# Kernel tuning notes

Hardware: AMD Instinct MI355X
Metric: run time of the kernel (lower is better)

Reference implementation:

```python
import jax, jax.numpy as jnp
import numpy as np

BATCH = 2
SEQ = 2048
DIM = 2048
HEADS = 16
DIM_HEAD = 64
DIM_INNER = HEADS * DIM_HEAD  # 1024
SOFTCAP = 50.0
EPS = 1e-12


def setup_inputs() -> dict:
    key = jax.random.key(0)
    k1, k2, k3, k4 = jax.random.split(key, 4)
    x = jax.random.normal(k1, (BATCH, SEQ, DIM), dtype=jnp.float32)
    # RMSNorm gamma param (initialized near zero in the torch module)
    gamma = jax.random.normal(k2, (DIM,), dtype=jnp.float32) * 0.02
    # Linear weights stored already-transposed: x @ W
    w_qkv = jax.random.normal(k3, (DIM, 3 * DIM_INNER), dtype=jnp.float32) * (DIM ** -0.5)
    w_out = jax.random.normal(k4, (DIM_INNER, DIM), dtype=jnp.float32) * (DIM_INNER ** -0.5)
    # (type, offset, length) triples per batch; bidirectional attention inside each span
    modalities = jnp.array(
        [[[0, 256, 256], [0, 1024, 512]],
         [[0, 128, 256], [0, 1536, 384]]], dtype=jnp.int32)
    return dict(x=x, gamma=gamma, w_qkv=w_qkv, w_out=w_out, modalities=modalities)


def _transfusion_attn_mask(seq_len, modalities):
    # causal | (q in span AND kv in span)  -> Bool[b, i, j]
    seq = jnp.arange(seq_len)
    causal = seq[:, None] >= seq[None, :]                      # [i, j]
    offsets = modalities[..., 1]                                # [b, m]
    ends = offsets + modalities[..., 2]                         # [b, m]
    q_in = seq[None, None, :] >= offsets[..., None]             # [b, m, i]
    kv_in = seq[None, None, :] < ends[..., None]                # [b, m, j]
    is_modality = jnp.any(q_in[..., :, None] & kv_in[..., None, :], axis=1)  # [b, i, j]
    return causal[None] | is_modality


def _rmsnorm(x, gamma):
    n = jnp.sqrt(jnp.sum(x * x, axis=-1, keepdims=True))
    x = x / jnp.maximum(n, EPS)
    return x * (DIM ** 0.5) * (gamma + 1.0)


def reference(x, gamma, w_qkv, w_out, modalities):
    xn = _rmsnorm(x, gamma)
    qkv = xn @ w_qkv                                            # [b, n, 3*h*d]
    qkv = qkv.reshape(BATCH, SEQ, 3, HEADS, DIM_HEAD)
    qkv = jnp.transpose(qkv, (2, 0, 3, 1, 4))                   # [3, b, h, n, d]
    q, k, v = qkv[0], qkv[1], qkv[2]
    q = q * (DIM_HEAD ** -0.5)
    sim = jnp.einsum('bhid,bhjd->bhij', q, k)
    sim = jnp.tanh(sim / SOFTCAP) * SOFTCAP                     # softclamp
    mask = _transfusion_attn_mask(SEQ, modalities)              # [b, i, j]
    neg = -jnp.finfo(sim.dtype).max
    sim = jnp.where(mask[:, None, :, :], sim, neg)
    attn = jax.nn.softmax(sim, axis=-1)
    out = jnp.einsum('bhij,bhjd->bhid', attn, v)
    out = jnp.transpose(out, (0, 2, 1, 3)).reshape(BATCH, SEQ, DIM_INNER)
    return out @ w_out
```

## Files before the change

### kernel.cpp

```cpp
#include <hip/hip_runtime.h>
#include <hip/hip_bf16.h>

typedef unsigned short u16;
typedef unsigned int u32;
typedef __attribute__((ext_vector_type(8))) short short8;
typedef __attribute__((ext_vector_type(4))) float f32x4;
typedef __attribute__((ext_vector_type(4))) u16 u16x4;

#define DEV __device__ __forceinline__

DEV u16 f2bf(float f) {
    union { float f; u32 u; } v; v.f = f;
    u32 r = v.u;
    u32 lsb = (r >> 16) & 1u;
    r += 0x7fffu + lsb;
    return (u16)(r >> 16);
}

DEV void gload_lds16(const u16* g, u16* l) {
    __builtin_amdgcn_global_load_lds(
        (const __attribute__((address_space(1))) u32*)(const void*)g,
        (__attribute__((address_space(3))) u32*)(void*)l,
        16, 0, 0);
}

__global__ void prep(const float* __restrict__ x, const float* __restrict__ gamma,
                     const float* __restrict__ w_qkv, const float* __restrict__ w_out,
                     u16* __restrict__ xn, u16* __restrict__ wqkvT, u16* __restrict__ woutT) {
    __shared__ float tile[32][33];
    __shared__ float red[4];
    int id = blockIdx.x;
    int t = threadIdx.x;
    if (id < 8192) {
        const float* in; u16* out; int R, C, bx, by;
        if (id < 6144) { in = w_qkv; out = wqkvT; R = 2048; C = 3072; bx = id % 96; by = id / 96; }
        else { id -= 6144; in = w_out; out = woutT; R = 1024; C = 2048; bx = id % 64; by = id / 64; }
        int tx = t & 31, ty = t >> 5;
        int c0 = bx * 32, r0 = by * 32;
#pragma unroll
        for (int i = 0; i < 4; i++)
            tile[ty * 4 + i][tx] = in[(size_t)(r0 + ty * 4 + i) * C + c0 + tx];
        __syncthreads();
#pragma unroll
        for (int i = 0; i < 4; i++)
            out[(size_t)(c0 + ty * 4 + i) * R + r0 + tx] = f2bf(tile[tx][ty * 4 + i]);
    } else {
        int row = id - 8192;
        const float4* xr = (const float4*)(x + (size_t)row * 2048);
        float4 a = xr[t];
        float4 b = xr[256 + t];
        float ss = a.x * a.x + a.y * a.y + a.z * a.z + a.w * a.w +
                   b.x * b.x + b.y * b.y + b.z * b.z + b.w * b.w;
#pragma unroll
        for (int off = 32; off; off >>= 1) ss += __shfl_xor(ss, off);
        if ((t & 63) == 0) red[t >> 6] = ss;
        __syncthreads();
        float tot = red[0] + red[1] + red[2] + red[3];
        float n = sqrtf(tot);
        float inv = 45.254833995939045f / fmaxf(n, 1e-12f);
        const float4* gr = (const float4*)gamma;
        float4 g0 = gr[t], g1 = gr[256 + t];
        u16x4 o0 = { f2bf(a.x * inv * (g0.x + 1.f)), f2bf(a.y * inv * (g0.y + 1.f)),
                     f2bf(a.z * inv * (g0.z + 1.f)), f2bf(a.w * inv * (g0.w + 1.f)) };
        u16x4 o1 = { f2bf(b.x * inv * (g1.x + 1.f)), f2bf(b.y * inv * (g1.y + 1.f)),
                     f2bf(b.z * inv * (g1.z + 1.f)), f2bf(b.w * inv * (g1.w + 1.f)) };
        u16x4* xo = (u16x4*)(xn + (size_t)row * 2048);
        xo[t] = o0;
        xo[256 + t] = o1;
    }
}

template <int EPI, int CCOL>
__global__ __launch_bounds__(512, 1) void gemm8f(
    const u16* __restrict__ A, const u16* __restrict__ BT,
    int M, int N, int K,
    float* __restrict__ Cout,
    u16* __restrict__ qb, u16* __restrict__ kb, u16* __restrict__ vT) {
    __shared__ __align__(16) u16 As[2][2][8192];
    __shared__ __align__(16) u16 Bs[2][2][8192];
    int t = threadIdx.x, lane = t & 63, wid = t >> 6;
    int g = lane >> 4, r = lane & 15;
    int wm = wid >> 2, wn = wid & 3;
    int rsw = r & 7;

    int id = blockIdx.x;
    int xcd = id & 7, slot = id >> 3;
    int by = (xcd >> 1) * 4 + slot / CCOL;
    int bx = (xcd & 1) * CCOL + slot % CCOL;
    int brow = by * 256, bcol = bx * 256;

    int gsl = (t & 7) ^ ((t >> 3) & 7);
    const u16* AgH = A + (size_t)(brow + (t >> 3)) * K + gsl * 8;
    const u16* BgH = BT + (size_t)(bcol + (t >> 3)) * K + gsl * 8;
    const size_t loK = (size_t)128 * K, r64K = (size_t)64 * K;
    int dstc = t * 8;

    f32x4 acc[2][4][2][2] = {};
    int NT = K >> 6;

#define STG_AH(bf_, kt_) { gload_lds16(AgH + (kt_) * 64, &As[bf_][0][dstc]); \
                           gload_lds16(AgH + r64K + (kt_) * 64, &As[bf_][0][dstc + 4096]); }
#define STG_AL(bf_, kt_) { gload_lds16(AgH + loK + (kt_) * 64, &As[bf_][1][dstc]); \
                           gload_lds16(AgH + loK + r64K + (kt_) * 64, &As[bf_][1][dstc + 4096]); }
#define STG_BH(bf_, kt_) { gload_lds16(BgH + (kt_) * 64, &Bs[bf_][0][dstc]); \
                           gload_lds16(BgH + r64K + (kt_) * 64, &Bs[bf_][0][dstc + 4096]); }
#define STG_BL(bf_, kt_) { gload_lds16(BgH + loK + (kt_) * 64, &Bs[bf_][1][dstc]); \
                           gload_lds16(BgH + loK + r64K + (kt_) * 64, &Bs[bf_][1][dstc + 4096]); }
#define READ_A(qm_) { \
    _Pragma("unroll") for (int mf = 0; mf < 4; mf++) \
    _Pragma("unroll") for (int ks = 0; ks < 2; ks++) \
        areg[mf][ks] = *(const short8*)&As[buf][qm_][(wm * 64 + mf * 16 + r) * 64 + (((ks << 2) + g) ^ rsw) * 8]; }
#define READ_B(qn_) { \
    _Pragma("unroll") for (int nf = 0; nf < 2; nf++) \
    _Pragma("unroll") for (int ks = 0; ks < 2; ks++) \
        breg[qn_][nf][ks] = *(const short8*)&Bs[buf][qn_][(wn * 32 + nf * 16 + r) * 64 + (((ks << 2) + g) ^ rsw) * 8]; }
#define PHASE_MFMA(qm_, qn_) { \
    __builtin_amdgcn_s_setprio(1); \
    _Pragma("unroll") for (int ks = 0; ks < 2; ks++) \
    _Pragma("unroll") for (int mf = 0; mf < 4; mf++) \
    _Pragma("unroll") for (int nf = 0; nf < 2; nf++) \
        acc[qm_][mf][qn_][nf] = __builtin_amdgcn_mfma_f32_16x16x32_bf16( \
            areg[mf][ks], breg[qn_][nf][ks], acc[qm_][mf][qn_][nf], 0, 0, 0); \
    __builtin_amdgcn_s_setprio(0); }
#define LGKM0() asm volatile("s_waitcnt lgkmcnt(0)" ::: "memory")
#define BAR() __builtin_amdgcn_s_barrier()

    STG_AH(0, 0); STG_AL(0, 0); STG_BH(0, 0); STG_BL(0, 0);
    asm volatile("s_waitcnt vmcnt(4)" ::: "memory");
    if (NT > 1) { STG_AH(1, 1); STG_AL(1, 1); STG_BH(1, 1); }
    asm volatile("s_waitcnt vmcnt(6)" ::: "memory");
    BAR();

    for (int kt = 0; kt < NT; ++kt) {
        int buf = kt & 1, ob = buf ^ 1;
        bool s1 = kt + 1 < NT, s2 = kt + 2 < NT;
        short8 areg[4][2], breg[2][2][2];

        READ_B(0); READ_A(0);
        if (s1) STG_BL(ob, kt + 1);
        BAR(); LGKM0();
        PHASE_MFMA(0, 0);
        BAR();

        READ_B(1);
        if (s2) STG_AH(buf, kt + 2);
        BAR(); LGKM0();
        PHASE_MFMA(0, 1);
        BAR();

        READ_A(1);
        if (s2) STG_AL(buf, kt + 2);
        BAR(); LGKM0();
        PHASE_MFMA(1, 0);
        BAR();

        if (s2) STG_BH(buf, kt + 2);
        PHASE_MFMA(1, 1);
        if (s2) { asm volatile("s_waitcnt vmcnt(6)" ::: "memory"); }
        else    { asm volatile("s_waitcnt vmcnt(0)" ::: "memory"); }
        BAR();
    }
#undef STG_AH
#undef STG_AL
#undef STG_BH
#undef STG_BL
#undef READ_A
#undef READ_B
#undef PHASE_MFMA
#undef LGKM0
#undef BAR

    if (EPI == 0) {
#pragma unroll
        for (int qm = 0; qm < 2; qm++)
#pragma unroll
            for (int mf = 0; mf < 4; mf++)
#pragma unroll
                for (int qn = 0; qn < 2; qn++)
#pragma unroll
                    for (int nf = 0; nf < 2; nf++) {
                        int cb = bcol + qn * 128 + wn * 32 + nf * 16 + r;
                        int which = cb >> 10;
                        int hd = cb & 1023;
                        int hh = hd >> 6, d = hd & 63;
#pragma unroll
                        for (int j = 0; j < 4; j++) {
                            int rr = brow + qm * 128 + wm * 64 + mf * 16 + 4 * g + j;
                            int b = rr >> 11, nn = rr & 2047;
                            float v = acc[qm][mf][qn][nf][j];
                            size_t bh = (size_t)(b * 16 + hh);
                            if (which == 0)      qb[(bh * 2048 + nn) * 64 + d] = f2bf(v * 0.125f);
                            else if (which == 1) kb[(bh * 2048 + nn) * 64 + d] = f2bf(v);
                            else                 vT[(bh * 64 + d) * 2048 + nn] = f2bf(v);
                        }
                    }
    } else {
#pragma unroll
        for (int qm = 0; qm < 2; qm++)
#pragma unroll
            for (int mf = 0; mf < 4; mf++)
#pragma unroll
                for (int qn = 0; qn < 2; qn++)
#pragma unroll
                    for (int nf = 0; nf < 2; nf++) {
                        int cb = bcol + qn * 128 + wn * 32 + nf * 16 + r;
#pragma unroll
                        for (int j = 0; j < 4; j++) {
                            int rr = brow + qm * 128 + wm * 64 + mf * 16 + 4 * g + j;
                            Cout[(size_t)rr * N + cb] = acc[qm][mf][qn][nf][j];
                        }
                    }
    }
}

__global__ __launch_bounds__(256, 3) void flash_attn(
    const u16* __restrict__ q, const u16* __restrict__ kk, const u16* __restrict__ vT,
    const int* __restrict__ mods, u16* __restrict__ attn_out) {
    __shared__ __align__(16) u16 Ks[2][4096];
    __shared__ __align__(16) u16 Vs[2][4096];
    __shared__ __align__(16) u16 Plds[4][16][72];
    int t = threadIdx.x, lane = t & 63, wave = t >> 6;
    int g = lane >> 4, r = lane & 15;
    int h = blockIdx.x, b = blockIdx.y;
    int qs = (31 - blockIdx.z) * 64;
    int bh = b * 16 + h;
    int qbase = qs + wave * 16;

    int off0 = mods[b * 6 + 1], end0 = off0 + mods[b * 6 + 2];
    int off1 = mods[b * 6 + 4], end1 = off1 + mods[b * 6 + 5];

    const u16* Qp = q + ((size_t)bh * 2048 + qbase) * 64;
    short8 qf0 = *(const short8*)(Qp + (size_t)r * 64 + 8 * g);
    short8 qf1 = *(const short8*)(Qp + (size_t)r * 64 + 32 + 8 * g);

    int iq = qbase + r;
    int lim0 = (iq >= off0) ? end0 : 0;
    int lim1 = (iq >= off1) ? end1 : 0;
    int rowlim = max(iq + 1, max(lim0, lim1));

    int jlb = qs + 64;
    if (qs + 63 >= off0) jlb = max(jlb, end0);
    if (qs + 63 >= off1) jlb = max(jlb, end1);

    const u16* Kp = kk + (size_t)bh * 2048 * 64;
    const u16* Vp = vT + (size_t)bh * 64 * 2048;
    u16* Pw = &Plds[wave][0][0];

    f32x4 ot[4] = {};
    float psA = 0.f, psB = 0.f;
    int sw = r & 7;

    auto stage64 = [&](const u16* gbase, int gstride, u16* lds) {
#pragma unroll
        for (int i = 0; i < 2; i++) {
            int c = i * 256 + t;
            int row = c >> 3;
            int gsl = (c & 7) ^ (row & 7);
            gload_lds16(gbase + (size_t)row * gstride + 8 * gsl,
                        lds + (size_t)(c & ~63) * 8);
        }
    };

    stage64(Kp, 64, Ks[0]);
    stage64(Vp, 2048, Vs[0]);
    int buf = 0;

    for (int jb = 0; jb < jlb; jb += 64) {
        if (jb + 64 < jlb) {
            stage64(Kp + (size_t)(jb + 64) * 64, 64, Ks[buf ^ 1]);
            stage64(Vp + (jb + 64), 2048, Vs[buf ^ 1]);
            asm volatile("s_waitcnt vmcnt(4)" ::: "memory");
        } else {
            asm volatile("s_waitcnt vmcnt(0)" ::: "memory");
        }
        __builtin_amdgcn_s_barrier();
        const u16* Kt = Ks[buf];
        const u16* Vt = Vs[buf];

        f32x4 st[4];
#pragma unroll
        for (int tt = 0; tt < 4; tt++) {
            int row = 16 * tt + r;
            short8 kf0 = *(const short8*)&Kt[(size_t)(row * 8 + (g ^ sw)) * 8];
            short8 kf1 = *(const short8*)&Kt[(size_t)(row * 8 + ((4 + g) ^ sw)) * 8];
            f32x4 z = {};
            z = __builtin_amdgcn_mfma_f32_16x16x32_bf16(kf0, qf0, z, 0, 0, 0);
            z = __builtin_amdgcn_mfma_f32_16x16x32_bf16(kf1, qf1, z, 0, 0, 0);
            st[tt] = z;
        }
#pragma unroll
        for (int tt = 0; tt < 4; tt++) {
            int kvb = jb + 16 * tt + 4 * g;
            float p0, p1, p2, p3;
#pragma unroll
            for (int j = 0; j < 4; j++) {
                float x = st[tt][j];
                float x2 = x * x;
                float inner = __builtin_fmaf(x2, 2.1333333e-8f, -1.3333333e-4f);
                float poly = __builtin_fmaf(x2, inner, 1.0f);
                float pv = __expf(x * poly);
                pv = (kvb + j < rowlim) ? pv : 0.f;
                if (j == 0) p0 = pv; else if (j == 1) p1 = pv;
                else if (j == 2) p2 = pv; else p3 = pv;
            }
            psA += p0 + p1;
            psB += p2 + p3;
            u32 pk0, pk1;
            asm("v_cvt_pk_bf16_f32 %0, %1, %2" : "=v"(pk0) : "v"(p0), "v"(p1));
            asm("v_cvt_pk_bf16_f32 %0, %1, %2" : "=v"(pk1) : "v"(p2), "v"(p3));
            *(u32*)&Pw[r * 72 + 16 * tt + 4 * g] = pk0;
            *(u32*)&Pw[r * 72 + 16 * tt + 4 * g + 2] = pk1;
        }
        short8 pf0 = *(const short8*)&Pw[r * 72 + 8 * g];
        short8 pf1 = *(const short8*)&Pw[r * 72 + 32 + 8 * g];
#pragma unroll
        for (int dt = 0; dt < 4; dt++) {
            int row = 16 * dt + r;
            short8 vf0 = *(const short8*)&Vt[(size_t)(row * 8 + (g ^ sw)) * 8];
            short8 vf1 = *(const short8*)&Vt[(size_t)(row * 8 + ((4 + g) ^ sw)) * 8];
            ot[dt] = __builtin_amdgcn_mfma_f32_16x16x32_bf16(vf0, pf0, ot[dt], 0, 0, 0);
            ot[dt] = __builtin_amdgcn_mfma_f32_16x16x32_bf16(vf1, pf1, ot[dt], 0, 0, 0);
        }
        asm volatile("s_waitcnt lgkmcnt(0)" ::: "memory");
        __builtin_amdgcn_s_barrier();
        buf ^= 1;
    }

    float lrow = psA + psB;
    lrow += __shfl_xor(lrow, 16);
    lrow += __shfl_xor(lrow, 32);
    float inv = 1.f / lrow;
    u16* Op = attn_out + ((size_t)(b * 2048 + qbase + r)) * 1024 + h * 64;
#pragma unroll
    for (int dt = 0; dt < 4; dt++) {
        u16x4 o = { f2bf(ot[dt][0] * inv), f2bf(ot[dt][1] * inv),
                    f2bf(ot[dt][2] * inv), f2bf(ot[dt][3] * inv) };
        *(u16x4*)(Op + dt * 16 + 4 * g) = o;
    }
}

extern "C" void kernel_launch(void* const* d_in, const int* in_sizes, int n_in,
                              void* d_out, int out_size, void* d_ws, size_t ws_size,
                              hipStream_t stream) {
    const float* x = (const float*)d_in[0];
    const float* gamma = (const float*)d_in[1];
    const float* w_qkv = (const float*)d_in[2];
    const float* w_out = (const float*)d_in[3];
    const int* mods = (const int*)d_in[4];
    float* out = (float*)d_out;

    u16* ws = (u16*)d_ws;
    u16* xn    = ws;
    u16* wqkvT = ws + 8388608;
    u16* woutT = ws + 14680064;
    u16* qb    = ws + 16777216;
    u16* kb    = ws + 20971520;
    u16* vT    = ws + 25165824;
    u16* ao    = ws + 29360128;

    prep<<<dim3(12288), dim3(256), 0, stream>>>(x, gamma, w_qkv, w_out, xn, wqkvT, woutT);
    gemm8f<0, 6><<<dim3(192), dim3(512), 0, stream>>>(xn, wqkvT, 4096, 3072, 2048,
                                                      nullptr, qb, kb, vT);
    flash_attn<<<dim3(16, 2, 32), dim3(256), 0, stream>>>(qb, kb, vT, mods, ao);
    gemm8f<1, 4><<<dim3(128), dim3(512), 0, stream>>>(ao, woutT, 4096, 2048, 1024,
                                                      out, nullptr, nullptr, nullptr);
}
```

Measured before the change: 177.5 us.

## Double-buffer GEMM register fragments to overlap LDS reads with MFMA

Restructures the GEMM main loop to ping-pong A/B register fragments (a0/a1, b0/b1). The next quarter's LDS reads are issued before the current MFMA phase, with partial lgkmcnt waits in place of full drains. This removes one barrier per phase and prefetches the next k-tile's first fragments during the last MFMA phase. The cost is higher register pressure, plus correctness that now depends on hand-tuned waitcnt counts and moved global-to-LDS staging points.

```diff
diff --git a/kernel.cpp b/kernel.cpp
--- a/kernel.cpp
+++ b/kernel.cpp
@@ -71,7 +71,7 @@
 }
 
 template <int EPI, int CCOL>
-__global__ __launch_bounds__(512, 1) void gemm8f(
+__global__ __launch_bounds__(512, 1) void gemmpp(
     const u16* __restrict__ A, const u16* __restrict__ BT,
     int M, int N, int K,
     float* __restrict__ Cout,
@@ -96,6 +96,7 @@
     int dstc = t * 8;
 
     f32x4 acc[2][4][2][2] = {};
+    short8 a0[4][2], a1[4][2], b0[2][2], b1[2][2];
     int NT = K >> 6;
 
 #define STG_AH(bf_, kt_) { gload_lds16(AgH + (kt_) * 64, &As[bf_][0][dstc]); \
@@ -106,68 +107,72 @@
                            gload_lds16(BgH + r64K + (kt_) * 64, &Bs[bf_][0][dstc + 4096]); }
 #define STG_BL(bf_, kt_) { gload_lds16(BgH + loK + (kt_) * 64, &Bs[bf_][1][dstc]); \
                            gload_lds16(BgH + loK + r64K + (kt_) * 64, &Bs[bf_][1][dstc + 4096]); }
-#define READ_A(qm_) { \
+#define RD_A(dst_, bb_, hh_) { \
     _Pragma("unroll") for (int mf = 0; mf < 4; mf++) \
     _Pragma("unroll") for (int ks = 0; ks < 2; ks++) \
-        areg[mf][ks] = *(const short8*)&As[buf][qm_][(wm * 64 + mf * 16 + r) * 64 + (((ks << 2) + g) ^ rsw) * 8]; }
-#define READ_B(qn_) { \
+        dst_[mf][ks] = *(const short8*)&As[bb_][hh_][(wm * 64 + mf * 16 + r) * 64 + (((ks << 2) + g) ^ rsw) * 8]; }
+#define RD_B(dst_, bb_, hh_) { \
     _Pragma("unroll") for (int nf = 0; nf < 2; nf++) \
     _Pragma("unroll") for (int ks = 0; ks < 2; ks++) \
-        breg[qn_][nf][ks] = *(const short8*)&Bs[buf][qn_][(wn * 32 + nf * 16 + r) * 64 + (((ks << 2) + g) ^ rsw) * 8]; }
-#define PHASE_MFMA(qm_, qn_) { \
+        dst_[nf][ks] = *(const short8*)&Bs[bb_][hh_][(wn * 32 + nf * 16 + r) * 64 + (((ks << 2) + g) ^ rsw) * 8]; }
+#define MFMA_Q(qm_, qn_, aa_, bb_) { \
     __builtin_amdgcn_s_setprio(1); \
     _Pragma("unroll") for (int ks = 0; ks < 2; ks++) \
     _Pragma("unroll") for (int mf = 0; mf < 4; mf++) \
     _Pragma("unroll") for (int nf = 0; nf < 2; nf++) \
         acc[qm_][mf][qn_][nf] = __builtin_amdgcn_mfma_f32_16x16x32_bf16( \
-            areg[mf][ks], breg[qn_][nf][ks], acc[qm_][mf][qn_][nf], 0, 0, 0); \
+            aa_[mf][ks], bb_[nf][ks], acc[qm_][mf][qn_][nf], 0, 0, 0); \
     __builtin_amdgcn_s_setprio(0); }
-#define LGKM0() asm volatile("s_waitcnt lgkmcnt(0)" ::: "memory")
+#define SCHEDB() __builtin_amdgcn_sched_barrier(0)
 #define BAR() __builtin_amdgcn_s_barrier()
 
     STG_AH(0, 0); STG_AL(0, 0); STG_BH(0, 0); STG_BL(0, 0);
-    asm volatile("s_waitcnt vmcnt(4)" ::: "memory");
     if (NT > 1) { STG_AH(1, 1); STG_AL(1, 1); STG_BH(1, 1); }
     asm volatile("s_waitcnt vmcnt(6)" ::: "memory");
+    SCHEDB();
     BAR();
+    RD_A(a0, 0, 0);
+    RD_B(b0, 0, 0);
 
     for (int kt = 0; kt < NT; ++kt) {
         int buf = kt & 1, ob = buf ^ 1;
         bool s1 = kt + 1 < NT, s2 = kt + 2 < NT;
-        short8 areg[4][2], breg[2][2][2];
-
-        READ_B(0); READ_A(0);
+
+        RD_B(b1, buf, 1);
         if (s1) STG_BL(ob, kt + 1);
-        BAR(); LGKM0();
-        PHASE_MFMA(0, 0);
+        asm volatile("s_waitcnt lgkmcnt(4)" ::: "memory");
+        SCHEDB();
+        MFMA_Q(0, 0, a0, b0);
         BAR();
 
-        READ_B(1);
+        RD_A(a1, buf, 1);
         if (s2) STG_AH(buf, kt + 2);
-        BAR(); LGKM0();
-        PHASE_MFMA(0, 1);
+        asm volatile("s_waitcnt lgkmcnt(8)" ::: "memory");
+        SCHEDB();
+        MFMA_Q(0, 1, a0, b1);
         BAR();
 
-        READ_A(1);
-        if (s2) STG_AL(buf, kt + 2);
-        BAR(); LGKM0();
-        PHASE_MFMA(1, 0);
+        asm volatile("s_waitcnt lgkmcnt(0)" ::: "memory");
+        SCHEDB();
+        MFMA_Q(1, 0, a1, b0);
         BAR();
 
-        if (s2) STG_BH(buf, kt + 2);
-        PHASE_MFMA(1, 1);
-        if (s2) { asm volatile("s_waitcnt vmcnt(6)" ::: "memory"); }
-        else    { asm volatile("s_waitcnt vmcnt(0)" ::: "memory"); }
+        if (s2) { STG_AL(buf, kt + 2); STG_BH(buf, kt + 2); }
+        if (s2)      { asm volatile("s_waitcnt vmcnt(6)" ::: "memory"); }
+        else if (s1) { asm volatile("s_waitcnt vmcnt(0)" ::: "memory"); }
+        SCHEDB();
+        if (s1) { RD_A(a0, ob, 0); RD_B(b0, ob, 0); }
+        MFMA_Q(1, 1, a1, b1);
         BAR();
     }
 #undef STG_AH
 #undef STG_AL
 #undef STG_BH
 #undef STG_BL
-#undef READ_A
-#undef READ_B
-#undef PHASE_MFMA
-#undef LGKM0
+#undef RD_A
+#undef RD_B
+#undef MFMA_Q
+#undef SCHEDB
 #undef BAR
 
     if (EPI == 0) {
@@ -359,9 +364,9 @@
     u16* ao    = ws + 29360128;
 
     prep<<<dim3(12288), dim3(256), 0, stream>>>(x, gamma, w_qkv, w_out, xn, wqkvT, woutT);
-    gemm8f<0, 6><<<dim3(192), dim3(512), 0, stream>>>(xn, wqkvT, 4096, 3072, 2048,
+    gemmpp<0, 6><<<dim3(192), dim3(512), 0, stream>>>(xn, wqkvT, 4096, 3072, 2048,
                                                       nullptr, qb, kb, vT);
     flash_attn<<<dim3(16, 2, 32), dim3(256), 0, stream>>>(qb, kb, vT, mods, ao);
-    gemm8f<1, 4><<<dim3(128), dim3(512), 0, stream>>>(ao, woutT, 4096, 2048, 1024,
+    gemmpp<1, 4><<<dim3(128), dim3(512), 0, stream>>>(ao, woutT, 4096, 2048, 1024,
                                                       out, nullptr, nullptr, nullptr);
 }
```

New measurement: 189.4 us. +6.7%, slower.
